# Performance work log

Hardware: AMD Instinct MI355X
Metric: run time of the kernel (lower is better)

Reference implementation:

```python
import jax, jax.numpy as jnp
import numpy as np

T = 16384       # tokens (flattened leading dims)
D_IN = 1024     # in_features
D_OUT = 1024    # out_features
E = 8           # n_models (experts)


def setup_inputs() -> dict:
    key = jax.random.key(0)
    kx, ki, kw, kb = jax.random.split(key, 4)
    x = jax.random.normal(kx, (T, D_IN), dtype=jnp.float32)
    idxs = jax.random.randint(ki, (T,), 0, E, dtype=jnp.int32)
    # Per-expert Linear params (nn.Linear default-ish init scale)
    scale = 1.0 / np.sqrt(D_IN)
    W = jax.random.uniform(kw, (E, D_IN, D_OUT), dtype=jnp.float32, minval=-scale, maxval=scale)
    b = jax.random.uniform(kb, (E, D_OUT), dtype=jnp.float32, minval=-scale, maxval=scale)
    return {"x": x, "idxs": idxs, "W": W, "b": b}


def reference(x, idxs, W, b):
    # Original: for each expert i, y[idxs==i] = Linear_i(x[idxs==i]); return relu(y).
    # Equivalent math: each token t gets expert idxs[t]'s linear.
    # Compute all experts densely (E is small), then gather the assigned row.
    ys = jnp.einsum('ti,eio->eto', x, W) + b[:, None, :]   # [E, T, D_OUT]
    y = ys[idxs, jnp.arange(x.shape[0])]                    # [T, D_OUT] pick assigned expert
    return jax.nn.relu(y)
```

## Files before the change

### kernel.cpp

```cpp
#include <hip/hip_runtime.h>
#include <hip/hip_bf16.h>
#include <stdint.h>


#define T_TOK 16384
#define DIN   1024
#define DOUT  1024
#define NE    8
#define BM    128
#define BN    128
#define BK    64
#define TPX   17
#define MAX_TILES 136
#define MP_MAX (T_TOK + NE * BM)

typedef __attribute__((ext_vector_type(8))) short short8;
typedef __attribute__((ext_vector_type(4))) short short4v;
typedef __attribute__((ext_vector_type(4))) float floatx4;
typedef __attribute__((ext_vector_type(4))) int int4v;

__device__ __forceinline__ short f2b(float f) {
  return __builtin_bit_cast(short, __float2bfloat16(f));
}
__device__ __forceinline__ float b2f(unsigned short u) {
  unsigned v = ((unsigned)u) << 16;
  return __builtin_bit_cast(float, v);
}
__device__ __forceinline__ void glds16(const void* g, void* l) {
  __builtin_amdgcn_global_load_lds(
      (__attribute__((address_space(1))) void*)g,
      (__attribute__((address_space(3))) void*)l, 16, 0, 0);
}

#define FLAG_OFF    0
#define NTILES_OFF  64
#define TABLE_OFF   1024
#define TPAD_OFF    8192
#define WT_OFF      81920
#define WS_NEED     (81920UL + (size_t)NE * DIN * DOUT * 2)

__global__ __launch_bounds__(1024) void k_front(
    const unsigned short* __restrict__ xu, const int* __restrict__ idxs,
    const void* __restrict__ Wsrc, short* __restrict__ Wt,
    int* __restrict__ flag, int* __restrict__ ntiles,
    int4v* __restrict__ table, int* __restrict__ tpad) {
  __shared__ int fS;
  __shared__ unsigned short tile[128][130];
  __shared__ int wtot[16][NE], waveBase[16][NE];
  __shared__ int totS[NE], padS[NE + 1];

  int tid = threadIdx.x;
  if (tid == 0) fS = 0;
  __syncthreads();
  if (tid < 256) {
    int ex = (xu[tid] >> 7) & 0xFF;
    if (ex >= 0xC0) atomicOr(&fS, 1);
  }
  __syncthreads();
  int fp32 = fS;

  if (blockIdx.x != 0) {
    int b = blockIdx.x - 1;
    int e = b >> 6, kt = (b >> 3) & 7, nt8 = b & 7;
    size_t ibase = (size_t)e * DIN * DOUT + (size_t)(kt * 128) * DOUT + nt8 * 128;
    int k = tid >> 3, n16 = (tid & 7) * 16;
    if (fp32) {
      const float* p = (const float*)Wsrc + ibase + (size_t)k * DOUT + n16;
      #pragma unroll
      for (int g = 0; g < 4; ++g) {
        floatx4 a = *(const floatx4*)(p + g * 4);
        #pragma unroll
        for (int j = 0; j < 4; ++j) tile[k][n16 + g * 4 + j] = (unsigned short)f2b(a[j]);
      }
    } else {
      const short* p = (const short*)Wsrc + ibase + (size_t)k * DOUT + n16;
      #pragma unroll
      for (int g = 0; g < 2; ++g) {
        short8 v = *(const short8*)(p + g * 8);
        #pragma unroll
        for (int j = 0; j < 8; ++j) tile[k][n16 + g * 8 + j] = (unsigned short)v[j];
      }
    }
    __syncthreads();
    int n = tid >> 3, k16 = (tid & 7) * 16;
    short8 o0, o1;
    #pragma unroll
    for (int j = 0; j < 8; ++j) {
      o0[j] = (short)tile[k16 + j][n];
      o1[j] = (short)tile[k16 + 8 + j][n];
    }
    size_t obase = (size_t)e * DOUT * DIN + (size_t)(nt8 * 128 + n) * DIN + kt * 128 + k16;
    *(short8*)(Wt + obase) = o0;
    *(short8*)(Wt + obase + 8) = o1;
    return;
  }

  int lane = tid & 63, w = tid >> 6;
  if (tid == 0) *flag = fp32;

  int c[NE];
  #pragma unroll
  for (int e = 0; e < NE; ++e) c[e] = 0;
  const int4v* iv = (const int4v*)idxs;
  int4v vv[4];
  #pragma unroll
  for (int it = 0; it < 4; ++it) {
    vv[it] = iv[tid * 4 + it];
    ++c[vv[it].x]; ++c[vv[it].y]; ++c[vv[it].z]; ++c[vv[it].w];
  }
  int incl[NE];
  #pragma unroll
  for (int e = 0; e < NE; ++e) {
    incl[e] = c[e];
    #pragma unroll
    for (int d = 1; d < 64; d <<= 1) {
      int o = __shfl_up(incl[e], d);
      if (lane >= d) incl[e] += o;
    }
  }
  if (lane == 63) {
    #pragma unroll
    for (int e = 0; e < NE; ++e) wtot[w][e] = incl[e];
  }
  __syncthreads();
  if (tid < NE) {
    int s = 0;
    for (int ww = 0; ww < 16; ++ww) s += wtot[ww][tid];
    totS[tid] = s;
  }
  __syncthreads();
  if (tid == 0) {
    int p = 0, tc = 0;
    for (int e = 0; e < NE; ++e) {
      padS[e] = p;
      int cn = totS[e];
      int nmt = (cn + BM - 1) >> 7;
      for (int m = 0; m < nmt; ++m) table[tc++] = (int4v){e, p + m * BM, 0, 0};
      p += nmt * BM;
    }
    padS[NE] = p;
    *ntiles = tc;
  }
  __syncthreads();
  if (tid < 128) {
    int ww = tid >> 3, e = tid & 7;
    int s = padS[e];
    for (int wp = 0; wp < ww; ++wp) s += wtot[wp][e];
    waveBase[ww][e] = s;
  }
  __syncthreads();
  int base[NE];
  #pragma unroll
  for (int e = 0; e < NE; ++e) base[e] = waveBase[w][e] + incl[e] - c[e];
  #pragma unroll
  for (int it = 0; it < 4; ++it) {
    #pragma unroll
    for (int cm = 0; cm < 4; ++cm) {
      int te = vv[it][cm];
      int tk = tid * 16 + it * 4 + cm;
      #pragma unroll
      for (int e0 = 0; e0 < NE; ++e0)
        if (te == e0) tpad[base[e0]++] = tk;
    }
  }
  #pragma unroll
  for (int e = 0; e < NE; ++e) {
    int start = padS[e] + totS[e];
    int len = padS[e + 1] - start;
    if (tid < len) tpad[start + tid] = -1;
  }
}

__launch_bounds__(256, 3)
__global__ void k_gemm(const void* __restrict__ xv, const void* __restrict__ bv,
                       const short* __restrict__ Wt, const int* __restrict__ tpad,
                       const int* __restrict__ ntilesp, const int4v* __restrict__ table,
                       const int* __restrict__ flagp, void* __restrict__ outv) {
  int bid = blockIdx.x;
  int xcd = bid & 7;
  int s = bid >> 3;
  int nt = s & 7;
  int ti = s >> 3;
  int t = xcd * TPX + ti;
  if (t >= *ntilesp) return;
  int4v te = table[t];
  int e = te.x, arow0 = te.y;
  int fp32 = *flagp;

  int tid = threadIdx.x;
  int lane = tid & 63;
  int wave = tid >> 6;

  __shared__ char lA[BM * BK * 4];
  __shared__ short lB[BN * BK];
  __shared__ int tokS[BM];

  if (tid < BM) tokS[tid] = tpad[arow0 + tid];
  __syncthreads();

  const short* WtE = Wt + (size_t)e * DOUT * DIN + (size_t)(nt * BN) * DIN;

  const short* bG[4];
  char* bL[4];
  #pragma unroll
  for (int s4 = 0; s4 < 4; ++s4) {
    int fl = tid + s4 * 256;
    int r = fl >> 3, p = fl & 7;
    int kc = p ^ (r & 7);
    bG[s4] = WtE + (size_t)r * DIN + kc * 8;
    bL[s4] = (char*)lB + (s4 * 256 + wave * 64) * 16;
  }

  int wm = wave & 1, wn = wave >> 1;
  int lrow = lane & 15, q = lane >> 4;
  int bOff[4][2];
  #pragma unroll
  for (int j = 0; j < 4; ++j) {
    int n = wn * 64 + j * 16 + lrow;
    #pragma unroll
    for (int h = 0; h < 2; ++h)
      bOff[j][h] = n * BK + (((h * 4 + q) ^ (n & 7)) * 8);
  }

  floatx4 acc[4][4];
  #pragma unroll
  for (int i = 0; i < 4; ++i)
    #pragma unroll
    for (int j = 0; j < 4; ++j)
      acc[i][j] = (floatx4){0.f, 0.f, 0.f, 0.f};

  if (fp32) {
    const char* aG[8];
    char* aL[8];
    #pragma unroll
    for (int s4 = 0; s4 < 8; ++s4) {
      int fl = tid + s4 * 256;
      int r = fl >> 4, p = fl & 15;
      int lc = p ^ (r & 15);
      int tok = tokS[r];
      if (tok < 0) tok = 0;
      aG[s4] = (const char*)xv + (size_t)tok * (DIN * 4) + lc * 16;
      aL[s4] = lA + (s4 * 256 + wave * 64) * 16;
    }
    int aOff[4][2];
    #pragma unroll
    for (int i = 0; i < 4; ++i) {
      int m = wm * 64 + i * 16 + lrow;
      #pragma unroll
      for (int h = 0; h < 2; ++h)
        aOff[i][h] = m * 256 + ((((h * 4 + q) * 2) ^ (m & 15)) * 16);
    }
    for (int k0 = 0; k0 < DIN; k0 += BK) {
      __syncthreads();
      #pragma unroll
      for (int s4 = 0; s4 < 4; ++s4) glds16(bG[s4] + k0, bL[s4]);
      #pragma unroll
      for (int s4 = 0; s4 < 8; ++s4) glds16(aG[s4] + k0 * 4, aL[s4]);
      __syncthreads();
      #pragma unroll
      for (int h = 0; h < 2; ++h) {
        short8 af[4], bf[4];
        #pragma unroll
        for (int i = 0; i < 4; ++i) {
          int a0 = aOff[i][h];
          floatx4 f0 = *(const floatx4*)(lA + a0);
          floatx4 f1 = *(const floatx4*)(lA + (a0 ^ 16));
          short8 v;
          v[0] = f2b(f0[0]); v[1] = f2b(f0[1]); v[2] = f2b(f0[2]); v[3] = f2b(f0[3]);
          v[4] = f2b(f1[0]); v[5] = f2b(f1[1]); v[6] = f2b(f1[2]); v[7] = f2b(f1[3]);
          af[i] = v;
        }
        #pragma unroll
        for (int j = 0; j < 4; ++j) bf[j] = *(const short8*)(lB + bOff[j][h]);
        #pragma unroll
        for (int i = 0; i < 4; ++i)
          #pragma unroll
          for (int j = 0; j < 4; ++j)
            acc[i][j] = __builtin_amdgcn_mfma_f32_16x16x32_bf16(bf[j], af[i], acc[i][j], 0, 0, 0);
      }
    }
  } else {
    const char* aG[4];
    char* aL[4];
    #pragma unroll
    for (int s4 = 0; s4 < 4; ++s4) {
      int fl = tid + s4 * 256;
      int r = fl >> 3, p = fl & 7;
      int kc = p ^ (r & 7);
      int tok = tokS[r];
      if (tok < 0) tok = 0;
      aG[s4] = (const char*)xv + (size_t)tok * (DIN * 2) + kc * 16;
      aL[s4] = lA + (s4 * 256 + wave * 64) * 16;
    }
    int aOff[4][2];
    #pragma unroll
    for (int i = 0; i < 4; ++i) {
      int m = wm * 64 + i * 16 + lrow;
      #pragma unroll
      for (int h = 0; h < 2; ++h)
        aOff[i][h] = m * BK + (((h * 4 + q) ^ (m & 7)) * 8);
    }
    for (int k0 = 0; k0 < DIN; k0 += BK) {
      __syncthreads();
      #pragma unroll
      for (int s4 = 0; s4 < 4; ++s4) glds16(bG[s4] + k0, bL[s4]);
      #pragma unroll
      for (int s4 = 0; s4 < 4; ++s4) glds16(aG[s4] + k0 * 2, aL[s4]);
      __syncthreads();
      #pragma unroll
      for (int h = 0; h < 2; ++h) {
        short8 af[4], bf[4];
        #pragma unroll
        for (int i = 0; i < 4; ++i) af[i] = *(const short8*)((const short*)lA + aOff[i][h]);
        #pragma unroll
        for (int j = 0; j < 4; ++j) bf[j] = *(const short8*)(lB + bOff[j][h]);
        #pragma unroll
        for (int i = 0; i < 4; ++i)
          #pragma unroll
          for (int j = 0; j < 4; ++j)
            acc[i][j] = __builtin_amdgcn_mfma_f32_16x16x32_bf16(bf[j], af[i], acc[i][j], 0, 0, 0);
      }
    }
  }

  #pragma unroll
  for (int i = 0; i < 4; ++i) {
    int tok = tokS[wm * 64 + i * 16 + lrow];
    if (tok < 0) continue;
    size_t rowb = (size_t)tok * DOUT + nt * BN + wn * 64 + q * 4;
    #pragma unroll
    for (int j = 0; j < 4; ++j) {
      int n = nt * BN + wn * 64 + j * 16 + q * 4;
      if (fp32) {
        floatx4 b4 = *(const floatx4*)((const float*)bv + e * DOUT + n);
        floatx4 o;
        #pragma unroll
        for (int r = 0; r < 4; ++r) {
          float v = acc[i][j][r] + b4[r];
          o[r] = v > 0.f ? v : 0.f;
        }
        *(floatx4*)((float*)outv + rowb + j * 16) = o;
      } else {
        short4v b4 = *(const short4v*)((const short*)bv + e * DOUT + n);
        short4v o;
        #pragma unroll
        for (int r = 0; r < 4; ++r) {
          float v = acc[i][j][r] + b2f((unsigned short)b4[r]);
          o[r] = f2b(v > 0.f ? v : 0.f);
        }
        *(short4v*)((short*)outv + rowb + j * 16) = o;
      }
    }
  }
}

__global__ void k_fallback(const void* __restrict__ xv, const int* __restrict__ idxs,
                           const void* __restrict__ Wv, const void* __restrict__ bv,
                           void* __restrict__ outv) {
  __shared__ float xrow[DIN];
  __shared__ int sflag;
  int t = blockIdx.x;
  int e = idxs[t];
  if (threadIdx.x == 0) {
    const unsigned short* u = (const unsigned short*)xv;
    int f = 0;
    for (int i = 0; i < 256; ++i) { int ex = (u[i] >> 7) & 0xFF; if (ex >= 0xC0) f = 1; }
    sflag = f;
  }
  __syncthreads();
  int fp32 = sflag;
  for (int i = threadIdx.x; i < DIN; i += 256)
    xrow[i] = fp32 ? ((const float*)xv)[(size_t)t * DIN + i]
                   : b2f(((const unsigned short*)xv)[(size_t)t * DIN + i]);
  __syncthreads();
  float a[4] = {0.f, 0.f, 0.f, 0.f};
  for (int k = 0; k < DIN; ++k) {
    float xk = xrow[k];
    size_t wb = (size_t)e * DIN * DOUT + (size_t)k * DOUT + threadIdx.x;
    #pragma unroll
    for (int j = 0; j < 4; ++j) {
      float w = fp32 ? ((const float*)Wv)[wb + j * 256]
                     : b2f(((const unsigned short*)Wv)[wb + j * 256]);
      a[j] += xk * w;
    }
  }
  #pragma unroll
  for (int j = 0; j < 4; ++j) {
    int n = threadIdx.x + j * 256;
    float bias = fp32 ? ((const float*)bv)[e * DOUT + n]
                      : b2f(((const unsigned short*)bv)[e * DOUT + n]);
    float v = a[j] + bias;
    v = v > 0.f ? v : 0.f;
    size_t o = (size_t)t * DOUT + n;
    if (fp32) ((float*)outv)[o] = v;
    else      ((short*)outv)[o] = f2b(v);
  }
}

extern "C" void kernel_launch(void* const* d_in, const int* in_sizes, int n_in,
                              void* d_out, int out_size, void* d_ws, size_t ws_size,
                              hipStream_t stream) {
  const void* x    = d_in[0];
  const int*  idxs = (const int*)d_in[1];
  const void* W    = d_in[2];
  const void* bias = d_in[3];

  if (ws_size < WS_NEED) {
    k_fallback<<<T_TOK, 256, 0, stream>>>(x, idxs, W, bias, d_out);
    return;
  }
  char* ws = (char*)d_ws;
  int* flag    = (int*)(ws + FLAG_OFF);
  int* ntiles  = (int*)(ws + NTILES_OFF);
  int4v* table = (int4v*)(ws + TABLE_OFF);
  int* tpad    = (int*)(ws + TPAD_OFF);
  short* Wt    = (short*)(ws + WT_OFF);

  k_front<<<1 + NE * 64, 1024, 0, stream>>>((const unsigned short*)x, idxs, W, Wt,
                                            flag, ntiles, table, tpad);
  k_gemm<<<8 * 8 * TPX, 256, 0, stream>>>(x, bias, Wt, tpad, ntiles, table, flag, d_out);
}
```

Baseline: 222.0 us.

## Pre-convert x to bf16 in front kernel and unify GEMM A-path

Adds extra blocks to the front kernel that convert the fp32 activations to a bf16 workspace copy, so the GEMM always streams bf16 A tiles instead of fp32 rows converted in registers. This halves A-tile global and LDS traffic per k-step, shrinks LDS for A, and lets occupancy rise to 4 blocks per CU. The cost is an extra full read of x plus a write and re-read of a bf16 copy, and a larger workspace requirement.

```diff
diff --git a/kernel.cpp b/kernel.cpp
--- a/kernel.cpp
+++ b/kernel.cpp
@@ -37,11 +37,15 @@
 #define TABLE_OFF   1024
 #define TPAD_OFF    8192
 #define WT_OFF      81920
-#define WS_NEED     (81920UL + (size_t)NE * DIN * DOUT * 2)
+#define XB_OFF      16859136
+#define WS_NEED     (16859136UL + (size_t)T_TOK * DIN * 2)
+
+#define TRANS_BLOCKS 512
+#define CONV_BLOCKS  1024
 
 __global__ __launch_bounds__(1024) void k_front(
     const unsigned short* __restrict__ xu, const int* __restrict__ idxs,
-    const void* __restrict__ Wsrc, short* __restrict__ Wt,
+    const void* __restrict__ Wsrc, short* __restrict__ Wt, short* __restrict__ xb,
     int* __restrict__ flag, int* __restrict__ ntiles,
     int4v* __restrict__ table, int* __restrict__ tpad) {
   __shared__ int fS;
@@ -58,6 +62,26 @@
   }
   __syncthreads();
   int fp32 = fS;
+
+  if (blockIdx.x >= 1 + TRANS_BLOCKS) {
+    if (!fp32) return;
+    int b2 = blockIdx.x - (1 + TRANS_BLOCKS);
+    size_t base = ((size_t)b2 * 1024 + tid) * 16;
+    const float* src = (const float*)xu + base;
+    floatx4 a0 = *(const floatx4*)(src + 0);
+    floatx4 a1 = *(const floatx4*)(src + 4);
+    floatx4 a2 = *(const floatx4*)(src + 8);
+    floatx4 a3 = *(const floatx4*)(src + 12);
+    short8 o0, o1;
+    #pragma unroll
+    for (int j = 0; j < 4; ++j) {
+      o0[j] = f2b(a0[j]); o0[4 + j] = f2b(a1[j]);
+      o1[j] = f2b(a2[j]); o1[4 + j] = f2b(a3[j]);
+    }
+    *(short8*)(xb + base) = o0;
+    *(short8*)(xb + base + 8) = o1;
+    return;
+  }
 
   if (blockIdx.x != 0) {
     int b = blockIdx.x - 1;
@@ -171,8 +195,9 @@
   }
 }
 
-__launch_bounds__(256, 3)
-__global__ void k_gemm(const void* __restrict__ xv, const void* __restrict__ bv,
+__launch_bounds__(256, 4)
+__global__ void k_gemm(const void* __restrict__ xv, const short* __restrict__ xb,
+                       const void* __restrict__ bv,
                        const short* __restrict__ Wt, const int* __restrict__ tpad,
                        const int* __restrict__ ntilesp, const int4v* __restrict__ table,
                        const int* __restrict__ flagp, void* __restrict__ outv) {
@@ -191,7 +216,7 @@
   int lane = tid & 63;
   int wave = tid >> 6;
 
-  __shared__ char lA[BM * BK * 4];
+  __shared__ short lA[BM * BK];
   __shared__ short lB[BN * BK];
   __shared__ int tokS[BM];
 
@@ -199,21 +224,34 @@
   __syncthreads();
 
   const short* WtE = Wt + (size_t)e * DOUT * DIN + (size_t)(nt * BN) * DIN;
-
+  const char* aBase = fp32 ? (const char*)xb : (const char*)xv;
+
+  const char* aG[4];
   const short* bG[4];
-  char* bL[4];
+  char *aL[4], *bL[4];
   #pragma unroll
   for (int s4 = 0; s4 < 4; ++s4) {
     int fl = tid + s4 * 256;
     int r = fl >> 3, p = fl & 7;
     int kc = p ^ (r & 7);
+    int tok = tokS[r];
+    if (tok < 0) tok = 0;
+    aG[s4] = aBase + (size_t)tok * (DIN * 2) + kc * 16;
+    aL[s4] = (char*)lA + (s4 * 256 + wave * 64) * 16;
     bG[s4] = WtE + (size_t)r * DIN + kc * 8;
     bL[s4] = (char*)lB + (s4 * 256 + wave * 64) * 16;
   }
 
   int wm = wave & 1, wn = wave >> 1;
   int lrow = lane & 15, q = lane >> 4;
-  int bOff[4][2];
+  int aOff[4][2], bOff[4][2];
+  #pragma unroll
+  for (int i = 0; i < 4; ++i) {
+    int m = wm * 64 + i * 16 + lrow;
+    #pragma unroll
+    for (int h = 0; h < 2; ++h)
+      aOff[i][h] = m * BK + (((h * 4 + q) ^ (m & 7)) * 8);
+  }
   #pragma unroll
   for (int j = 0; j < 4; ++j) {
     int n = wn * 64 + j * 16 + lrow;
@@ -229,97 +267,25 @@
     for (int j = 0; j < 4; ++j)
       acc[i][j] = (floatx4){0.f, 0.f, 0.f, 0.f};
 
-  if (fp32) {
-    const char* aG[8];
-    char* aL[8];
-    #pragma unroll
-    for (int s4 = 0; s4 < 8; ++s4) {
-      int fl = tid + s4 * 256;
-      int r = fl >> 4, p = fl & 15;
-      int lc = p ^ (r & 15);
-      int tok = tokS[r];
-      if (tok < 0) tok = 0;
-      aG[s4] = (const char*)xv + (size_t)tok * (DIN * 4) + lc * 16;
-      aL[s4] = lA + (s4 * 256 + wave * 64) * 16;
-    }
-    int aOff[4][2];
-    #pragma unroll
-    for (int i = 0; i < 4; ++i) {
-      int m = wm * 64 + i * 16 + lrow;
-      #pragma unroll
-      for (int h = 0; h < 2; ++h)
-        aOff[i][h] = m * 256 + ((((h * 4 + q) * 2) ^ (m & 15)) * 16);
-    }
-    for (int k0 = 0; k0 < DIN; k0 += BK) {
-      __syncthreads();
-      #pragma unroll
-      for (int s4 = 0; s4 < 4; ++s4) glds16(bG[s4] + k0, bL[s4]);
-      #pragma unroll
-      for (int s4 = 0; s4 < 8; ++s4) glds16(aG[s4] + k0 * 4, aL[s4]);
-      __syncthreads();
-      #pragma unroll
-      for (int h = 0; h < 2; ++h) {
-        short8 af[4], bf[4];
-        #pragma unroll
-        for (int i = 0; i < 4; ++i) {
-          int a0 = aOff[i][h];
-          floatx4 f0 = *(const floatx4*)(lA + a0);
-          floatx4 f1 = *(const floatx4*)(lA + (a0 ^ 16));
-          short8 v;
-          v[0] = f2b(f0[0]); v[1] = f2b(f0[1]); v[2] = f2b(f0[2]); v[3] = f2b(f0[3]);
-          v[4] = f2b(f1[0]); v[5] = f2b(f1[1]); v[6] = f2b(f1[2]); v[7] = f2b(f1[3]);
-          af[i] = v;
-        }
-        #pragma unroll
-        for (int j = 0; j < 4; ++j) bf[j] = *(const short8*)(lB + bOff[j][h]);
-        #pragma unroll
-        for (int i = 0; i < 4; ++i)
-          #pragma unroll
-          for (int j = 0; j < 4; ++j)
-            acc[i][j] = __builtin_amdgcn_mfma_f32_16x16x32_bf16(bf[j], af[i], acc[i][j], 0, 0, 0);
-      }
-    }
-  } else {
-    const char* aG[4];
-    char* aL[4];
-    #pragma unroll
-    for (int s4 = 0; s4 < 4; ++s4) {
-      int fl = tid + s4 * 256;
-      int r = fl >> 3, p = fl & 7;
-      int kc = p ^ (r & 7);
-      int tok = tokS[r];
-      if (tok < 0) tok = 0;
-      aG[s4] = (const char*)xv + (size_t)tok * (DIN * 2) + kc * 16;
-      aL[s4] = lA + (s4 * 256 + wave * 64) * 16;
-    }
-    int aOff[4][2];
-    #pragma unroll
-    for (int i = 0; i < 4; ++i) {
-      int m = wm * 64 + i * 16 + lrow;
-      #pragma unroll
-      for (int h = 0; h < 2; ++h)
-        aOff[i][h] = m * BK + (((h * 4 + q) ^ (m & 7)) * 8);
-    }
-    for (int k0 = 0; k0 < DIN; k0 += BK) {
-      __syncthreads();
-      #pragma unroll
-      for (int s4 = 0; s4 < 4; ++s4) glds16(bG[s4] + k0, bL[s4]);
-      #pragma unroll
-      for (int s4 = 0; s4 < 4; ++s4) glds16(aG[s4] + k0 * 2, aL[s4]);
-      __syncthreads();
-      #pragma unroll
-      for (int h = 0; h < 2; ++h) {
-        short8 af[4], bf[4];
-        #pragma unroll
-        for (int i = 0; i < 4; ++i) af[i] = *(const short8*)((const short*)lA + aOff[i][h]);
-        #pragma unroll
-        for (int j = 0; j < 4; ++j) bf[j] = *(const short8*)(lB + bOff[j][h]);
-        #pragma unroll
-        for (int i = 0; i < 4; ++i)
-          #pragma unroll
-          for (int j = 0; j < 4; ++j)
-            acc[i][j] = __builtin_amdgcn_mfma_f32_16x16x32_bf16(bf[j], af[i], acc[i][j], 0, 0, 0);
-      }
+  for (int k0 = 0; k0 < DIN; k0 += BK) {
+    __syncthreads();
+    #pragma unroll
+    for (int s4 = 0; s4 < 4; ++s4) glds16(bG[s4] + k0, bL[s4]);
+    #pragma unroll
+    for (int s4 = 0; s4 < 4; ++s4) glds16(aG[s4] + k0 * 2, aL[s4]);
+    __syncthreads();
+    #pragma unroll
+    for (int h = 0; h < 2; ++h) {
+      short8 af[4], bf[4];
+      #pragma unroll
+      for (int i = 0; i < 4; ++i) af[i] = *(const short8*)(lA + aOff[i][h]);
+      #pragma unroll
+      for (int j = 0; j < 4; ++j) bf[j] = *(const short8*)(lB + bOff[j][h]);
+      #pragma unroll
+      for (int i = 0; i < 4; ++i)
+        #pragma unroll
+        for (int j = 0; j < 4; ++j)
+          acc[i][j] = __builtin_amdgcn_mfma_f32_16x16x32_bf16(bf[j], af[i], acc[i][j], 0, 0, 0);
     }
   }
 
@@ -415,8 +381,9 @@
   int4v* table = (int4v*)(ws + TABLE_OFF);
   int* tpad    = (int*)(ws + TPAD_OFF);
   short* Wt    = (short*)(ws + WT_OFF);
-
-  k_front<<<1 + NE * 64, 1024, 0, stream>>>((const unsigned short*)x, idxs, W, Wt,
-                                            flag, ntiles, table, tpad);
-  k_gemm<<<8 * 8 * TPX, 256, 0, stream>>>(x, bias, Wt, tpad, ntiles, table, flag, d_out);
-}
+  short* xb    = (short*)(ws + XB_OFF);
+
+  k_front<<<1 + TRANS_BLOCKS + CONV_BLOCKS, 1024, 0, stream>>>(
+      (const unsigned short*)x, idxs, W, Wt, xb, flag, ntiles, table, tpad);
+  k_gemm<<<8 * 8 * TPX, 256, 0, stream>>>(x, xb, bias, Wt, tpad, ntiles, table, flag, d_out);
+}
```

After: 202.0 us. -9.0%, faster.
